# Kernel optimization log

Hardware: AMD Instinct MI355X
Metric: run time of the kernel (lower is better)

The kernel has to match this reference:

```python
import jax, jax.numpy as jnp
import numpy as np

B, N, F, T = 32, 2048, 16, 64


def setup_inputs() -> dict:
    key = jax.random.key(0)
    ks = jax.random.split(key, 6)
    return {
        "x": jax.random.normal(ks[0], (B, N, F, T), dtype=jnp.float32),
        "U1": jax.random.normal(ks[1], (N, 1), dtype=jnp.float32) * (1.0 / np.sqrt(N)),
        "U2": jax.random.normal(ks[2], (F, N), dtype=jnp.float32) * (1.0 / np.sqrt(F)),
        "U3": jax.random.normal(ks[3], (1, F), dtype=jnp.float32) * (1.0 / np.sqrt(F)),
        "be": jax.random.normal(ks[4], (1, T, T), dtype=jnp.float32),
        "Ve": jax.random.normal(ks[5], (T, T), dtype=jnp.float32) * (1.0 / np.sqrt(T)),
    }


def reference(x, U1, U2, U3, be, Ve):
    # x: (B, N, F, T)
    # lhs = squeeze(x^T(0,3,2,1) @ U1) @ U2 : contract N then project F->N -> (B, T, N)
    lhs = jnp.einsum("bnft,n->btf", x, U1[:, 0]) @ U2  # (B, T, N)
    # rhs = squeeze(U3 @ x, -2): contract F -> (B, N, T)
    rhs = jnp.einsum("f,bnft->bnt", U3[0], x)  # (B, N, T)
    product = jnp.matmul(lhs, rhs)  # (B, T, T)
    E = jnp.einsum("ts,bsu->btu", Ve, jax.nn.sigmoid(product + be))  # (B, T, T)
    return jax.nn.softmax(E, axis=1)
```

## Files before the change

### kernel.cpp

```cpp
#include <hip/hip_runtime.h>
#include <hip/hip_bf16.h>
#include <math.h>


#define B_ 32
#define N_ 2048
#define F_ 16
#define T_ 64
#define NPB 128
#define CHUNKS (N_ / NPB)

__global__ __launch_bounds__(256) void ta_pass1(
    const float* __restrict__ x, const float* __restrict__ U1,
    const float* __restrict__ U2, const float* __restrict__ U3,
    float* __restrict__ partial)
{
  const int blk    = blockIdx.x;
  const int b      = blk / CHUNKS;
  const int chunk  = blk % CHUNKS;
  const int n_base = chunk * NPB;
  const int tid    = threadIdx.x;
  const int tp     = tid & 31;
  const int n_sub  = tid >> 5;

  __shared__ float u1s[NPB];
  __shared__ float u2s[F_][NPB];
  __shared__ float red[4 * 2048];

  for (int i = tid; i < NPB; i += 256) u1s[i] = U1[n_base + i];
  for (int i = tid; i < F_ * NPB; i += 256) {
    int f = i / NPB, nl = i % NPB;
    u2s[f][nl] = U2[f * N_ + n_base + nl];
  }
  float u3r[F_];
  #pragma unroll
  for (int f = 0; f < F_; ++f) u3r[f] = U3[f];
  __syncthreads();

  float2 ya[F_], za[F_];
  #pragma unroll
  for (int f = 0; f < F_; ++f) {
    ya[f] = make_float2(0.f, 0.f);
    za[f] = make_float2(0.f, 0.f);
  }

  const float* xb = x + ((size_t)b * N_ + n_base) * (F_ * T_);
  for (int it = 0; it < NPB / 8; ++it) {
    const int nl = n_sub + it * 8;
    const float* xn = xb + (size_t)nl * (F_ * T_) + 2 * tp;
    const float u1 = u1s[nl];
    float r0 = 0.f, r1 = 0.f;
    #pragma unroll
    for (int f = 0; f < F_; ++f) {
      float2 v = *reinterpret_cast<const float2*>(xn + f * T_);
      ya[f].x = fmaf(u1, v.x, ya[f].x);
      ya[f].y = fmaf(u1, v.y, ya[f].y);
      r0 = fmaf(u3r[f], v.x, r0);
      r1 = fmaf(u3r[f], v.y, r1);
    }
    #pragma unroll
    for (int f = 0; f < F_; ++f) {
      const float u2 = u2s[f][nl];
      za[f].x = fmaf(u2, r0, za[f].x);
      za[f].y = fmaf(u2, r1, za[f].y);
    }
  }

  #pragma unroll
  for (int f = 0; f < F_; ++f) {
    ya[f].x += __shfl_xor(ya[f].x, 32);
    ya[f].y += __shfl_xor(ya[f].y, 32);
    za[f].x += __shfl_xor(za[f].x, 32);
    za[f].y += __shfl_xor(za[f].y, 32);
  }
  const int lane = tid & 63, w = tid >> 6;
  if (lane < 32) {
    #pragma unroll
    for (int f = 0; f < F_; ++f) {
      red[w * 2048 + (f * 2 + 0) * 32 + tp]        = ya[f].x;
      red[w * 2048 + (f * 2 + 1) * 32 + tp]        = ya[f].y;
      red[w * 2048 + (32 + f * 2 + 0) * 32 + tp]   = za[f].x;
      red[w * 2048 + (32 + f * 2 + 1) * 32 + tp]   = za[f].y;
    }
  }
  __syncthreads();
  float* pb = partial + (size_t)blk * 2048;
  #pragma unroll
  for (int k = 0; k < 8; ++k) {
    int idx = tid + k * 256;
    pb[idx] = red[idx] + red[2048 + idx] + red[4096 + idx] + red[6144 + idx];
  }
}

__global__ __launch_bounds__(256) void ta_finish(
    const float* __restrict__ partial, const float* __restrict__ be,
    const float* __restrict__ Ve, float* __restrict__ out)
{
  const int b = blockIdx.x;
  const int tid = threadIdx.x;
  __shared__ float ys[T_][F_ + 1];
  __shared__ float zs[F_][T_ + 1];
  __shared__ float sig[T_][T_ + 1];
  __shared__ float Es[T_][T_ + 1];

  #pragma unroll
  for (int k = 0; k < 8; ++k) {
    const int idx = tid + k * 256;
    float s = 0.f;
    for (int j = 0; j < CHUNKS; ++j)
      s += partial[((size_t)b * CHUNKS + j) * 2048 + idx];
    const int vi = idx >> 5, tp = idx & 31;
    if (vi < 32) { int f = vi >> 1, c = vi & 1; ys[2 * tp + c][f] = s; }
    else { int v2 = vi - 32; int f = v2 >> 1, c = v2 & 1; zs[f][2 * tp + c] = s; }
  }
  __syncthreads();

  const int t  = tid >> 2;
  const int ub = (tid & 3) * 16;
  #pragma unroll
  for (int i = 0; i < 16; ++i) {
    const int u = ub + i;
    float acc = 0.f;
    #pragma unroll
    for (int f = 0; f < F_; ++f) acc = fmaf(ys[t][f], zs[f][u], acc);
    acc += be[t * T_ + u];
    sig[t][u] = 1.f / (1.f + __expf(-acc));
  }
  __syncthreads();
  #pragma unroll
  for (int i = 0; i < 16; ++i) {
    const int u = ub + i;
    float acc = 0.f;
    #pragma unroll
    for (int s = 0; s < T_; ++s) acc = fmaf(Ve[t * T_ + s], sig[s][u], acc);
    Es[t][u] = acc;
  }
  __syncthreads();

  if (tid < T_) {
    const int u = tid;
    float m = -INFINITY;
    for (int t2 = 0; t2 < T_; ++t2) m = fmaxf(m, Es[t2][u]);
    float den = 0.f;
    for (int t2 = 0; t2 < T_; ++t2) den += __expf(Es[t2][u] - m);
    const float inv = 1.f / den;
    for (int t2 = 0; t2 < T_; ++t2)
      out[(size_t)b * T_ * T_ + t2 * T_ + u] = __expf(Es[t2][u] - m) * inv;
  }
}

extern "C" void kernel_launch(void* const* d_in, const int* in_sizes, int n_in,
                              void* d_out, int out_size, void* d_ws, size_t ws_size,
                              hipStream_t stream) {
  const float* x  = (const float*)d_in[0];
  const float* U1 = (const float*)d_in[1];
  const float* U2 = (const float*)d_in[2];
  const float* U3 = (const float*)d_in[3];
  const float* be = (const float*)d_in[4];
  const float* Ve = (const float*)d_in[5];
  float* out = (float*)d_out;
  float* partial = (float*)d_ws;

  ta_pass1<<<B_ * CHUNKS, 256, 0, stream>>>(x, U1, U2, U3, partial);
  ta_finish<<<B_, 256, 0, stream>>>(partial, be, Ve, out);
}
```

Baseline: 76.33 us.

## Halve per-block N chunk, use float4 loads, defer U2 projection to LDS pass

Each pass1 block now covers 64 nodes instead of 128, which doubles the grid. Threads load x as float4 instead of float2. The F-contracted rhs values are staged in LDS and the U2 projection is done afterwards as a small per-block matmul, so the main loop keeps fewer register accumulators. The finish kernel reads partials as float4 and spreads the softmax over all 256 threads with shuffle reductions. The cost is twice as many partials for the finish kernel to reduce.

```diff
diff --git a/kernel.cpp b/kernel.cpp
--- a/kernel.cpp
+++ b/kernel.cpp
@@ -7,7 +7,7 @@
 #define N_ 2048
 #define F_ 16
 #define T_ 64
-#define NPB 128
+#define NPB 64
 #define CHUNKS (N_ / NPB)
 
 __global__ __launch_bounds__(256) void ta_pass1(
@@ -20,75 +20,92 @@
   const int chunk  = blk % CHUNKS;
   const int n_base = chunk * NPB;
   const int tid    = threadIdx.x;
-  const int tp     = tid & 31;
-  const int n_sub  = tid >> 5;
-
-  __shared__ float u1s[NPB];
-  __shared__ float u2s[F_][NPB];
-  __shared__ float red[4 * 2048];
-
-  for (int i = tid; i < NPB; i += 256) u1s[i] = U1[n_base + i];
-  for (int i = tid; i < F_ * NPB; i += 256) {
-    int f = i / NPB, nl = i % NPB;
-    u2s[f][nl] = U2[f * N_ + n_base + nl];
+  const int tp     = tid & 15;
+  const int n_sub  = tid >> 4;
+  const int w      = tid >> 6;
+  const int lane   = tid & 63;
+
+  __shared__ float  u1s[NPB];
+  __shared__ float  u2t[NPB][F_ + 1];
+  __shared__ float4 rlds[NPB][16];
+  __shared__ float4 red[4][256];
+
+  if (tid < NPB) u1s[tid] = U1[n_base + tid];
+  for (int i = tid; i < NPB * F_; i += 256) {
+    const int f = i >> 6, n = i & 63;
+    u2t[n][f] = U2[f * N_ + n_base + n];
   }
   float u3r[F_];
   #pragma unroll
   for (int f = 0; f < F_; ++f) u3r[f] = U3[f];
   __syncthreads();
 
-  float2 ya[F_], za[F_];
-  #pragma unroll
-  for (int f = 0; f < F_; ++f) {
-    ya[f] = make_float2(0.f, 0.f);
-    za[f] = make_float2(0.f, 0.f);
-  }
+  float4 ya[F_];
+  #pragma unroll
+  for (int f = 0; f < F_; ++f) ya[f] = make_float4(0.f, 0.f, 0.f, 0.f);
 
   const float* xb = x + ((size_t)b * N_ + n_base) * (F_ * T_);
-  for (int it = 0; it < NPB / 8; ++it) {
-    const int nl = n_sub + it * 8;
-    const float* xn = xb + (size_t)nl * (F_ * T_) + 2 * tp;
+  #pragma unroll
+  for (int it = 0; it < NPB / 16; ++it) {
+    const int nl = n_sub + it * 16;
+    const float* xn = xb + (size_t)nl * (F_ * T_) + 4 * tp;
     const float u1 = u1s[nl];
-    float r0 = 0.f, r1 = 0.f;
+    float4 r = make_float4(0.f, 0.f, 0.f, 0.f);
     #pragma unroll
     for (int f = 0; f < F_; ++f) {
-      float2 v = *reinterpret_cast<const float2*>(xn + f * T_);
+      const float4 v = *reinterpret_cast<const float4*>(xn + f * T_);
       ya[f].x = fmaf(u1, v.x, ya[f].x);
       ya[f].y = fmaf(u1, v.y, ya[f].y);
-      r0 = fmaf(u3r[f], v.x, r0);
-      r1 = fmaf(u3r[f], v.y, r1);
-    }
-    #pragma unroll
-    for (int f = 0; f < F_; ++f) {
-      const float u2 = u2s[f][nl];
-      za[f].x = fmaf(u2, r0, za[f].x);
-      za[f].y = fmaf(u2, r1, za[f].y);
-    }
+      ya[f].z = fmaf(u1, v.z, ya[f].z);
+      ya[f].w = fmaf(u1, v.w, ya[f].w);
+      r.x = fmaf(u3r[f], v.x, r.x);
+      r.y = fmaf(u3r[f], v.y, r.y);
+      r.z = fmaf(u3r[f], v.z, r.z);
+      r.w = fmaf(u3r[f], v.w, r.w);
+    }
+    rlds[nl][tp] = r;
   }
 
   #pragma unroll
   for (int f = 0; f < F_; ++f) {
+    ya[f].x += __shfl_xor(ya[f].x, 16);
+    ya[f].y += __shfl_xor(ya[f].y, 16);
+    ya[f].z += __shfl_xor(ya[f].z, 16);
+    ya[f].w += __shfl_xor(ya[f].w, 16);
     ya[f].x += __shfl_xor(ya[f].x, 32);
     ya[f].y += __shfl_xor(ya[f].y, 32);
-    za[f].x += __shfl_xor(za[f].x, 32);
-    za[f].y += __shfl_xor(za[f].y, 32);
-  }
-  const int lane = tid & 63, w = tid >> 6;
-  if (lane < 32) {
-    #pragma unroll
-    for (int f = 0; f < F_; ++f) {
-      red[w * 2048 + (f * 2 + 0) * 32 + tp]        = ya[f].x;
-      red[w * 2048 + (f * 2 + 1) * 32 + tp]        = ya[f].y;
-      red[w * 2048 + (32 + f * 2 + 0) * 32 + tp]   = za[f].x;
-      red[w * 2048 + (32 + f * 2 + 1) * 32 + tp]   = za[f].y;
-    }
-  }
-  __syncthreads();
-  float* pb = partial + (size_t)blk * 2048;
-  #pragma unroll
-  for (int k = 0; k < 8; ++k) {
-    int idx = tid + k * 256;
-    pb[idx] = red[idx] + red[2048 + idx] + red[4096 + idx] + red[6144 + idx];
+    ya[f].z += __shfl_xor(ya[f].z, 32);
+    ya[f].w += __shfl_xor(ya[f].w, 32);
+  }
+  if ((lane >> 4) == 0) {
+    #pragma unroll
+    for (int f = 0; f < F_; ++f) red[w][f * 16 + tp] = ya[f];
+  }
+  __syncthreads();
+
+  float4* pb = reinterpret_cast<float4*>(partial + (size_t)blk * 2048);
+  {
+    const float4 a = red[0][tid], c = red[1][tid], d = red[2][tid], e = red[3][tid];
+    float4 yv;
+    yv.x = a.x + c.x + d.x + e.x;
+    yv.y = a.y + c.y + d.y + e.y;
+    yv.z = a.z + c.z + d.z + e.z;
+    yv.w = a.w + c.w + d.w + e.w;
+    pb[tid] = yv;
+  }
+  {
+    const int f = tid >> 4, uq = tid & 15;
+    float4 zv = make_float4(0.f, 0.f, 0.f, 0.f);
+    #pragma unroll
+    for (int n = 0; n < NPB; ++n) {
+      const float  u2 = u2t[n][f];
+      const float4 r  = rlds[n][uq];
+      zv.x = fmaf(u2, r.x, zv.x);
+      zv.y = fmaf(u2, r.y, zv.y);
+      zv.z = fmaf(u2, r.z, zv.z);
+      zv.w = fmaf(u2, r.w, zv.w);
+    }
+    pb[256 + tid] = zv;
   }
 }
 
@@ -96,35 +113,46 @@
     const float* __restrict__ partial, const float* __restrict__ be,
     const float* __restrict__ Ve, float* __restrict__ out)
 {
-  const int b = blockIdx.x;
+  const int b   = blockIdx.x;
   const int tid = threadIdx.x;
   __shared__ float ys[T_][F_ + 1];
-  __shared__ float zs[F_][T_ + 1];
+  __shared__ float zs[F_][T_];
   __shared__ float sig[T_][T_ + 1];
   __shared__ float Es[T_][T_ + 1];
 
-  #pragma unroll
-  for (int k = 0; k < 8; ++k) {
-    const int idx = tid + k * 256;
-    float s = 0.f;
-    for (int j = 0; j < CHUNKS; ++j)
-      s += partial[((size_t)b * CHUNKS + j) * 2048 + idx];
-    const int vi = idx >> 5, tp = idx & 31;
-    if (vi < 32) { int f = vi >> 1, c = vi & 1; ys[2 * tp + c][f] = s; }
-    else { int v2 = vi - 32; int f = v2 >> 1, c = v2 & 1; zs[f][2 * tp + c] = s; }
-  }
-  __syncthreads();
-
-  const int t  = tid >> 2;
+  const float4* p4 = reinterpret_cast<const float4*>(partial) + (size_t)b * CHUNKS * 512;
+  #pragma unroll
+  for (int k = 0; k < 2; ++k) {
+    const int i4 = tid + k * 256;
+    float4 s = make_float4(0.f, 0.f, 0.f, 0.f);
+    #pragma unroll 4
+    for (int j = 0; j < CHUNKS; ++j) {
+      const float4 v = p4[(size_t)j * 512 + i4];
+      s.x += v.x; s.y += v.y; s.z += v.z; s.w += v.w;
+    }
+    if (i4 < 256) {
+      const int f = i4 >> 4, t0 = (i4 & 15) * 4;
+      ys[t0 + 0][f] = s.x; ys[t0 + 1][f] = s.y;
+      ys[t0 + 2][f] = s.z; ys[t0 + 3][f] = s.w;
+    } else {
+      const int j4 = i4 - 256;
+      const int f = j4 >> 4, u0 = (j4 & 15) * 4;
+      zs[f][u0 + 0] = s.x; zs[f][u0 + 1] = s.y;
+      zs[f][u0 + 2] = s.z; zs[f][u0 + 3] = s.w;
+    }
+  }
+  __syncthreads();
+
+  const int tr = tid >> 2;
   const int ub = (tid & 3) * 16;
   #pragma unroll
   for (int i = 0; i < 16; ++i) {
     const int u = ub + i;
     float acc = 0.f;
     #pragma unroll
-    for (int f = 0; f < F_; ++f) acc = fmaf(ys[t][f], zs[f][u], acc);
-    acc += be[t * T_ + u];
-    sig[t][u] = 1.f / (1.f + __expf(-acc));
+    for (int f = 0; f < F_; ++f) acc = fmaf(ys[tr][f], zs[f][u], acc);
+    acc += be[tr * T_ + u];
+    sig[tr][u] = 1.f / (1.f + __expf(-acc));
   }
   __syncthreads();
   #pragma unroll
@@ -132,21 +160,27 @@
     const int u = ub + i;
     float acc = 0.f;
     #pragma unroll
-    for (int s = 0; s < T_; ++s) acc = fmaf(Ve[t * T_ + s], sig[s][u], acc);
-    Es[t][u] = acc;
-  }
-  __syncthreads();
-
-  if (tid < T_) {
-    const int u = tid;
-    float m = -INFINITY;
-    for (int t2 = 0; t2 < T_; ++t2) m = fmaxf(m, Es[t2][u]);
-    float den = 0.f;
-    for (int t2 = 0; t2 < T_; ++t2) den += __expf(Es[t2][u] - m);
-    const float inv = 1.f / den;
-    for (int t2 = 0; t2 < T_; ++t2)
-      out[(size_t)b * T_ * T_ + t2 * T_ + u] = __expf(Es[t2][u] - m) * inv;
-  }
+    for (int s = 0; s < T_; ++s) acc = fmaf(Ve[tr * T_ + s], sig[s][u], acc);
+    Es[tr][u] = acc;
+  }
+  __syncthreads();
+
+  const int u = tid >> 2, p = tid & 3;
+  float m = -INFINITY;
+  #pragma unroll
+  for (int r = 0; r < 16; ++r) m = fmaxf(m, Es[p * 16 + r][u]);
+  m = fmaxf(m, __shfl_xor(m, 1));
+  m = fmaxf(m, __shfl_xor(m, 2));
+  float den = 0.f;
+  #pragma unroll
+  for (int r = 0; r < 16; ++r) den += __expf(Es[p * 16 + r][u] - m);
+  den += __shfl_xor(den, 1);
+  den += __shfl_xor(den, 2);
+  const float inv = 1.f / den;
+  #pragma unroll
+  for (int r = 0; r < 16; ++r)
+    out[(size_t)b * T_ * T_ + (p * 16 + r) * T_ + u] =
+        __expf(Es[p * 16 + r][u] - m) * inv;
 }
 
 extern "C" void kernel_launch(void* const* d_in, const int* in_sizes, int n_in,
```

Result: no change. 77.17 us (+1.1%).
